# Kernel optimization log

Measured on AMD Instinct MI355X. Metric: run time of the kernel, lower is better.

Reference implementation:

```python
import jax, jax.numpy as jnp
import numpy as np


def setup_inputs() -> dict:
    key = jax.random.key(0)
    k1, k2, k3 = jax.random.split(key, 3)
    B, C, H, W = 8, 128, 256, 256
    K = 7
    x = jax.random.normal(k1, (B, C, H, W), dtype=jnp.float32)
    # PyTorch Conv2d default init: U(-b, b), b = 1/sqrt(fan_in), fan_in = 1*K*K
    bound = 1.0 / np.sqrt(K * K)
    conv_w = jax.random.uniform(k2, (1, 1, K, K), minval=-bound, maxval=bound, dtype=jnp.float32)
    conv_b = jax.random.uniform(k3, (1,), minval=-bound, maxval=bound, dtype=jnp.float32)
    return {"input": x, "conv_w": conv_w, "conv_b": conv_b}


def reference(input, conv_w, conv_b):
    # ChannelPool: max over channel dim, keep dim -> [B,1,H,W]
    pooled = jnp.max(input, axis=1, keepdims=True)
    # 7x7 conv (1->1), stride 1, pad 3 (SAME for odd kernel)
    conv = jax.lax.conv_general_dilated(
        pooled, conv_w,
        window_strides=(1, 1), padding=[(3, 3), (3, 3)],
        dimension_numbers=("NCHW", "OIHW", "NCHW"),
    ) + conv_b[None, :, None, None]
    attn = jax.nn.sigmoid(conv)  # [B,1,H,W]
    return input * attn  # broadcast over channels
```

## Files before the change

kernel.cpp:

```cpp
#include <hip/hip_runtime.h>

#define Bc 8
#define Cc 128
#define Hc 256
#define Wc 256
#define HWc (Hc * Wc)
#define CHWc (Cc * HWc)

typedef float floatx4 __attribute__((ext_vector_type(4)));

__global__ void __launch_bounds__(256) channel_max_kernel(const float* __restrict__ in,
                                                          float* __restrict__ pooled) {
    int tid = blockIdx.x * blockDim.x + threadIdx.x;
    int e = tid << 2;
    int b = e >> 16;
    int s = e & (HWc - 1);
    const floatx4* base = (const floatx4*)(in + (size_t)b * CHWc + s);
    const int cstride = HWc / 4;

    floatx4 m0 = base[0];
    floatx4 m1 = base[(size_t)cstride];
    floatx4 m2 = base[(size_t)(2 * cstride)];
    floatx4 m3 = base[(size_t)(3 * cstride)];
#pragma unroll 4
    for (int c = 4; c < Cc; c += 4) {
        floatx4 v0 = base[(size_t)c * cstride];
        floatx4 v1 = base[(size_t)(c + 1) * cstride];
        floatx4 v2 = base[(size_t)(c + 2) * cstride];
        floatx4 v3 = base[(size_t)(c + 3) * cstride];
        m0.x = fmaxf(m0.x, v0.x); m0.y = fmaxf(m0.y, v0.y);
        m0.z = fmaxf(m0.z, v0.z); m0.w = fmaxf(m0.w, v0.w);
        m1.x = fmaxf(m1.x, v1.x); m1.y = fmaxf(m1.y, v1.y);
        m1.z = fmaxf(m1.z, v1.z); m1.w = fmaxf(m1.w, v1.w);
        m2.x = fmaxf(m2.x, v2.x); m2.y = fmaxf(m2.y, v2.y);
        m2.z = fmaxf(m2.z, v2.z); m2.w = fmaxf(m2.w, v2.w);
        m3.x = fmaxf(m3.x, v3.x); m3.y = fmaxf(m3.y, v3.y);
        m3.z = fmaxf(m3.z, v3.z); m3.w = fmaxf(m3.w, v3.w);
    }
    m0.x = fmaxf(m0.x, m1.x); m0.y = fmaxf(m0.y, m1.y);
    m0.z = fmaxf(m0.z, m1.z); m0.w = fmaxf(m0.w, m1.w);
    m2.x = fmaxf(m2.x, m3.x); m2.y = fmaxf(m2.y, m3.y);
    m2.z = fmaxf(m2.z, m3.z); m2.w = fmaxf(m2.w, m3.w);
    floatx4 m;
    m.x = fmaxf(m0.x, m2.x); m.y = fmaxf(m0.y, m2.y);
    m.z = fmaxf(m0.z, m2.z); m.w = fmaxf(m0.w, m2.w);
    ((floatx4*)pooled)[tid] = m;
}

__global__ void __launch_bounds__(256) conv_sigmoid_kernel(const float* __restrict__ pooled,
                                                           const float* __restrict__ wgt,
                                                           const float* __restrict__ bias,
                                                           float* __restrict__ attn) {
    __shared__ float wsm[49];
    if (threadIdx.x < 49) wsm[threadIdx.x] = wgt[threadIdx.x];
    __syncthreads();

    int tid = blockIdx.x * blockDim.x + threadIdx.x;
    int b = tid / HWc;
    int s = tid - b * HWc;
    int h = s >> 8;
    int w = s & (Wc - 1);
    const float* p = pooled + b * HWc;

    float acc = bias[0];
#pragma unroll
    for (int i = 0; i < 7; ++i) {
        int hh = h - 3 + i;
        if ((unsigned)hh < (unsigned)Hc) {
            const float* row = p + hh * Wc;
#pragma unroll
            for (int j = 0; j < 7; ++j) {
                int ww = w - 3 + j;
                if ((unsigned)ww < (unsigned)Wc) {
                    acc = fmaf(row[ww], wsm[i * 7 + j], acc);
                }
            }
        }
    }
    attn[tid] = 1.0f / (1.0f + expf(-acc));
}

#define K3_CPT 8
__global__ void __launch_bounds__(256) mul_kernel(const float* __restrict__ in,
                                                  const float* __restrict__ attn,
                                                  float* __restrict__ out) {
    unsigned rb = gridDim.x - 1u - blockIdx.x;
    unsigned t = rb * blockDim.x + threadIdx.x;
    unsigned pos = t & (Bc * HWc / 4 - 1);
    unsigned g = t >> 17;
    unsigned e = pos << 2;
    unsigned b = e >> 16;
    unsigned s = e & (HWc - 1);

    floatx4 a = ((const floatx4*)attn)[pos];

    const size_t base = (size_t)b * CHWc + (size_t)(g * K3_CPT) * HWc + s;
    const float* ip = in + base;
    float* op = out + base;

    floatx4 v[K3_CPT];
#pragma unroll
    for (int k = 0; k < K3_CPT; ++k)
        v[k] = *(const floatx4*)(ip + (size_t)k * HWc);
#pragma unroll
    for (int k = 0; k < K3_CPT; ++k) {
        v[k].x *= a.x;
        v[k].y *= a.y;
        v[k].z *= a.z;
        v[k].w *= a.w;
        __builtin_nontemporal_store(v[k], (floatx4*)(op + (size_t)k * HWc));
    }
}

extern "C" void kernel_launch(void* const* d_in, const int* in_sizes, int n_in,
                              void* d_out, int out_size, void* d_ws, size_t ws_size,
                              hipStream_t stream) {
    const float* input  = (const float*)d_in[0];
    const float* conv_w = (const float*)d_in[1];
    const float* conv_b = (const float*)d_in[2];
    float* out = (float*)d_out;

    float* pooled = (float*)d_ws;
    float* attn   = pooled + (size_t)Bc * HWc;

    channel_max_kernel<<<(Bc * HWc / 4) / 256, 256, 0, stream>>>(input, pooled);

    conv_sigmoid_kernel<<<(Bc * HWc) / 256, 256, 0, stream>>>(pooled, conv_w, conv_b, attn);

    mul_kernel<<<(Bc * HWc / 4) * (Cc / K3_CPT) / 256, 256, 0, stream>>>(input, attn, out);
}
```

Measured before the change: 498.2 us.

## Process batch in chunks so multiply pass rereads input from cache

Splits the batch into chunks of four images and runs max-pool, conv-sigmoid and multiply per chunk. The aim is that each chunk's input stays resident in the last-level cache between the channel-max read and the multiply read, removing a second full HBM read. The multiply kernel is also simplified to one vector per thread, dropping the reversed block order and the per-thread channel batching. This adds kernel launches and smaller grids per launch.

```diff
diff --git a/kernel.cpp b/kernel.cpp
--- a/kernel.cpp
+++ b/kernel.cpp
@@ -7,15 +7,19 @@
 #define HWc (Hc * Wc)
 #define CHWc (Cc * HWc)
 
+#define IMGS 4
+#define NCHUNK (Bc / IMGS)
+
 typedef float floatx4 __attribute__((ext_vector_type(4)));
 
 __global__ void __launch_bounds__(256) channel_max_kernel(const float* __restrict__ in,
-                                                          float* __restrict__ pooled) {
+                                                          float* __restrict__ pooled,
+                                                          int b0) {
     int tid = blockIdx.x * blockDim.x + threadIdx.x;
     int e = tid << 2;
-    int b = e >> 16;
+    int bl = e >> 16;
     int s = e & (HWc - 1);
-    const floatx4* base = (const floatx4*)(in + (size_t)b * CHWc + s);
+    const floatx4* base = (const floatx4*)(in + (size_t)(b0 + bl) * CHWc + s);
     const int cstride = HWc / 4;
 
     floatx4 m0 = base[0];
@@ -44,23 +48,24 @@
     floatx4 m;
     m.x = fmaxf(m0.x, m2.x); m.y = fmaxf(m0.y, m2.y);
     m.z = fmaxf(m0.z, m2.z); m.w = fmaxf(m0.w, m2.w);
-    ((floatx4*)pooled)[tid] = m;
+    ((floatx4*)(pooled + (size_t)b0 * HWc))[tid] = m;
 }
 
 __global__ void __launch_bounds__(256) conv_sigmoid_kernel(const float* __restrict__ pooled,
                                                            const float* __restrict__ wgt,
                                                            const float* __restrict__ bias,
-                                                           float* __restrict__ attn) {
+                                                           float* __restrict__ attn,
+                                                           int b0) {
     __shared__ float wsm[49];
     if (threadIdx.x < 49) wsm[threadIdx.x] = wgt[threadIdx.x];
     __syncthreads();
 
     int tid = blockIdx.x * blockDim.x + threadIdx.x;
-    int b = tid / HWc;
-    int s = tid - b * HWc;
+    int bl = tid >> 16;
+    int s = tid & (HWc - 1);
     int h = s >> 8;
     int w = s & (Wc - 1);
-    const float* p = pooled + b * HWc;
+    const float* p = pooled + (size_t)(b0 + bl) * HWc;
 
     float acc = bias[0];
 #pragma unroll
@@ -77,39 +82,27 @@
             }
         }
     }
-    attn[tid] = 1.0f / (1.0f + expf(-acc));
+    attn[(size_t)(b0 + bl) * HWc + s] = 1.0f / (1.0f + expf(-acc));
 }
 
-#define K3_CPT 8
 __global__ void __launch_bounds__(256) mul_kernel(const float* __restrict__ in,
                                                   const float* __restrict__ attn,
-                                                  float* __restrict__ out) {
-    unsigned rb = gridDim.x - 1u - blockIdx.x;
-    unsigned t = rb * blockDim.x + threadIdx.x;
-    unsigned pos = t & (Bc * HWc / 4 - 1);
-    unsigned g = t >> 17;
-    unsigned e = pos << 2;
-    unsigned b = e >> 16;
-    unsigned s = e & (HWc - 1);
+                                                  float* __restrict__ out,
+                                                  int b0) {
+    unsigned t = blockIdx.x * blockDim.x + threadIdx.x;
+    unsigned e = t << 2;
+    unsigned bl = e >> 23;
+    unsigned rem = e & (CHWc - 1);
+    unsigned s = rem & (HWc - 1);
+    size_t idx = (size_t)(b0 + bl) * CHWc + rem;
 
-    floatx4 a = ((const floatx4*)attn)[pos];
-
-    const size_t base = (size_t)b * CHWc + (size_t)(g * K3_CPT) * HWc + s;
-    const float* ip = in + base;
-    float* op = out + base;
-
-    floatx4 v[K3_CPT];
-#pragma unroll
-    for (int k = 0; k < K3_CPT; ++k)
-        v[k] = *(const floatx4*)(ip + (size_t)k * HWc);
-#pragma unroll
-    for (int k = 0; k < K3_CPT; ++k) {
-        v[k].x *= a.x;
-        v[k].y *= a.y;
-        v[k].z *= a.z;
-        v[k].w *= a.w;
-        __builtin_nontemporal_store(v[k], (floatx4*)(op + (size_t)k * HWc));
-    }
+    floatx4 v = *(const floatx4*)(in + idx);
+    floatx4 a = *(const floatx4*)(attn + (size_t)(b0 + bl) * HWc + s);
+    v.x *= a.x;
+    v.y *= a.y;
+    v.z *= a.z;
+    v.w *= a.w;
+    __builtin_nontemporal_store(v, (floatx4*)(out + idx));
 }
 
 extern "C" void kernel_launch(void* const* d_in, const int* in_sizes, int n_in,
@@ -123,9 +116,11 @@
     float* pooled = (float*)d_ws;
     float* attn   = pooled + (size_t)Bc * HWc;
 
-    channel_max_kernel<<<(Bc * HWc / 4) / 256, 256, 0, stream>>>(input, pooled);
-
-    conv_sigmoid_kernel<<<(Bc * HWc) / 256, 256, 0, stream>>>(pooled, conv_w, conv_b, attn);
-
-    mul_kernel<<<(Bc * HWc / 4) * (Cc / K3_CPT) / 256, 256, 0, stream>>>(input, attn, out);
+    for (int c = 0; c < NCHUNK; ++c) {
+        int b0 = c * IMGS;
+        channel_max_kernel<<<(IMGS * HWc / 4) / 256, 256, 0, stream>>>(input, pooled, b0);
+        conv_sigmoid_kernel<<<(IMGS * HWc) / 256, 256, 0, stream>>>(pooled, conv_w, conv_b,
+                                                                    attn, b0);
+        mul_kernel<<<(IMGS * CHWc / 4) / 256, 256, 0, stream>>>(input, attn, out, b0);
+    }
 }
```

New measurement: 493.5 us. Within noise of the previous version (-0.9%).
